# Performance work log

Hardware: AMD Instinct MI355X
Metric: run time of the kernel (lower is better)

The kernel has to match this reference:

```python
import jax, jax.numpy as jnp
import numpy as np

TAU = 0.5

def _l2norm(x, eps=1e-12):
    n = jnp.linalg.norm(x, axis=-1, keepdims=True)
    return x / jnp.maximum(n, eps)

def _gat(a, idx):
    # per-rating gather: a [R, N, ...], idx [R, E] -> [R, E, ...]
    return jax.vmap(lambda x, j: x[j])(a, idx)

def setup_inputs() -> dict:
    key = jax.random.key(0)
    R, Nu, Nm, E, F, d, Dr, OUT = 5, 50000, 20000, 100000, 4, 16, 64, 64
    ks = jax.random.split(key, 17)
    inp = {
        "user_feat_k": jax.random.normal(ks[0], (R, Nu, d), jnp.float32),
        "movie_feat_k": jax.random.normal(ks[1], (R, Nm, d), jnp.float32),
        "user_feat_sum": 0.1 * jax.random.normal(ks[2], (R, Nu, F, d), jnp.float32),
        "movie_feat_sum": 0.1 * jax.random.normal(ks[3], (R, Nm, F, d), jnp.float32),
        "review_feat": 0.1 * jax.random.normal(ks[4], (R, E, F, Dr), jnp.float32),
        "prototypes": 0.1 * jax.random.normal(ks[5], (F, Dr), jnp.float32),
        "eta": jax.random.normal(ks[6], (R, E), jnp.float32),
        "node_w_fwd": 0.25 * jax.random.normal(ks[7], (R, d, d), jnp.float32),
        "review_w_fwd": 0.1 * jax.random.normal(ks[8], (R, d, Dr), jnp.float32),
        "node_w_rev": 0.25 * jax.random.normal(ks[9], (R, d, d), jnp.float32),
        "review_w_rev": 0.1 * jax.random.normal(ks[10], (R, d, Dr), jnp.float32),
        "ufc_w": 0.25 * jax.random.normal(ks[11], (OUT, d), jnp.float32),
        "ufc_b": jnp.zeros((OUT,), jnp.float32),
        "ifc_w": 0.25 * jax.random.normal(ks[12], (OUT, d), jnp.float32),
        "ifc_b": jnp.zeros((OUT,), jnp.float32),
        "edges_u": jax.random.randint(ks[13], (R, E), 0, Nu, jnp.int64),
        "edges_m": jax.random.randint(ks[14], (R, E), 0, Nm, jnp.int64),
        "k": 1,
    }
    return inp

def reference(user_feat_k, movie_feat_k, user_feat_sum, movie_feat_sum,
              review_feat, prototypes, eta, node_w_fwd, review_w_fwd,
              node_w_rev, review_w_rev, ufc_w, ufc_b, ifc_w, ifc_b,
              edges_u, edges_m, k):
    R, E = edges_u.shape
    Nu = user_feat_k.shape[1]
    Nm = movie_feat_k.shape[1]

    # ---- per-edge contrastive weights (vectorized over R ratings) ----
    row_feat = _l2norm(_gat(user_feat_k, edges_u))          # [R,E,d]
    col_feat = _l2norm(_gat(movie_feat_k, edges_m))         # [R,E,d]
    sim_k = (row_feat * col_feat).sum(-1) / TAU             # [R,E]
    sim_all = (_gat(user_feat_sum, edges_u) * _gat(movie_feat_sum, edges_m)).sum(-1) / TAU  # [R,E,F]
    exp_sim = jnp.exp(sim_k) / jnp.exp(sim_all).sum(-1)

    rf_k = review_feat[:, :, k, :]                          # [R,E,Dr]
    ad_k = jnp.einsum('red,d->re', rf_k, prototypes[k]) / TAU
    ad_all = jnp.einsum('refd,fd->ref', review_feat, prototypes) / TAU
    exp_anchor = jnp.exp(ad_k) / jnp.exp(ad_all).sum(-1)

    g = jax.nn.sigmoid(eta[:, :E])                          # eta[rating][:E]
    w = g * exp_anchor + (1.0 - g) * exp_sim                # [R,E]

    # ---- scatter-normalize (fwd + rev etypes give identical w, so the
    #      original's (sum over both)/2 equals a single-direction sum) ----
    norm_user = jax.ops.segment_sum(w.reshape(-1), edges_u.reshape(-1), num_segments=Nu)
    norm_movie = jax.ops.segment_sum(w.reshape(-1), edges_m.reshape(-1), num_segments=Nm)
    n_ij = jnp.sqrt(norm_user[edges_u] * norm_movie[edges_m])  # [R,E]
    w_norm = w / n_ij
    int_dist = w_norm.reshape(R * E, 1)                     # movie->user etypes, rating order

    # ---- GCMC hetero conv: gather src, add projected review feat, scale, scatter ----
    hu = jnp.einsum('rnd,rod->rno', user_feat_k, node_w_fwd)     # node_w per fwd etype
    rfp_f = jnp.einsum('red,rod->reo', rf_k, review_w_fwd)
    msg_m = (_gat(hu, edges_u) + rfp_f) * w_norm[..., None]      # [R,E,d]
    ifeat = jax.ops.segment_sum(msg_m.reshape(R * E, -1), edges_m.reshape(-1), num_segments=Nm)

    hm = jnp.einsum('rnd,rod->rno', movie_feat_k, node_w_rev)    # node_w per rev etype
    rfp_r = jnp.einsum('red,rod->reo', rf_k, review_w_rev)
    msg_u = (_gat(hm, edges_m) + rfp_r) * w_norm[..., None]
    ufeat = jax.ops.segment_sum(msg_u.reshape(R * E, -1), edges_u.reshape(-1), num_segments=Nu)

    lrelu = lambda x: jnp.where(x >= 0, x, 0.1 * x)
    ufeat = lrelu(ufeat) @ ufc_w.T + ufc_b
    ifeat = lrelu(ifeat) @ ifc_w.T + ifc_b
    return (ufeat, ifeat, int_dist)
```

## Files before the change

kernel.cpp:

```cpp
#include <hip/hip_runtime.h>
#include <hip/hip_bf16.h>

#define TAU_INV 2.0f
#define R_ 5
#define NU 50000
#define NM 20000
#define EDGES 100000
#define F_ 4
#define D_ 16
#define DR 64
#define OUT_ 64
#define EPW 32

typedef __attribute__((ext_vector_type(8))) short short8;
typedef __attribute__((ext_vector_type(4))) float f32x4;

__device__ __forceinline__ float dot4(float4 a, float4 b) {
    return a.x * b.x + a.y * b.y + a.z * b.z + a.w * b.w;
}

__device__ __forceinline__ ushort f2bf(float x) {
    __hip_bfloat16 h = __float2bfloat16(x);
    return *reinterpret_cast<ushort*>(&h);
}

__device__ __forceinline__ short8 pack8(float4 lo, float4 hi) {
    short8 v;
    v[0] = (short)f2bf(lo.x); v[1] = (short)f2bf(lo.y);
    v[2] = (short)f2bf(lo.z); v[3] = (short)f2bf(lo.w);
    v[4] = (short)f2bf(hi.x); v[5] = (short)f2bf(hi.y);
    v[6] = (short)f2bf(hi.z); v[7] = (short)f2bf(hi.w);
    return v;
}

__global__ __launch_bounds__(256) void k_edge_w(
    const float* __restrict__ ufk, const float* __restrict__ mfk,
    const float* __restrict__ ufs, const float* __restrict__ mfs,
    const float* __restrict__ rfeat, const float* __restrict__ proto,
    const float* __restrict__ eta, const int* __restrict__ eu,
    const int* __restrict__ em, const int* __restrict__ kp,
    float* __restrict__ wbuf, float* __restrict__ nrm_u, float* __restrict__ nrm_m)
{
    const int tid = threadIdx.x;
    const int wv = tid >> 6, l = tid & 63;
    const int g16 = l >> 4;
    const int j   = l & 15;
    const int r = blockIdx.y;
    int e = (blockIdx.x * 4 + wv) * 4 + g16;
    const bool live = (e < EDGES);
    if (e >= EDGES) e = EDGES - 1;
    const int idx = r * EDGES + e;
    const int u = eu[idx], m = em[idx];
    const int kk = kp[0];

    const float4 pu = ((const float4*)(ufs + (size_t)(r * NU + u) * 64))[j];
    const float4 pm = ((const float4*)(mfs + (size_t)(r * NM + m) * 64))[j];
    float p = dot4(pu, pm);
    p += __shfl_xor(p, 1); p += __shfl_xor(p, 2);
    const float es = expf(p * TAU_INV);
    float dsim = es;
    dsim += __shfl_xor(dsim, 4); dsim += __shfl_xor(dsim, 8);

    const int jc = j & 3;
    const float4 u4 = ((const float4*)(ufk + (size_t)(r * NU + u) * 16))[jc];
    const float4 m4 = ((const float4*)(mfk + (size_t)(r * NM + m) * 16))[jc];
    float su = dot4(u4, u4), sm = dot4(m4, m4), sd = dot4(u4, m4);
    su += __shfl_xor(su, 1); su += __shfl_xor(su, 2);
    sm += __shfl_xor(sm, 1); sm += __shfl_xor(sm, 2);
    sd += __shfl_xor(sd, 1); sd += __shfl_xor(sd, 2);
    const float nsim = expf(sd / (fmaxf(sqrtf(su), 1e-12f) * fmaxf(sqrtf(sm), 1e-12f)) * TAU_INV);

    const float4* rf4 = (const float4*)(rfeat + (size_t)idx * 256);
    const float4* pr4 = (const float4*)proto;
    const int base = (j >> 2) * 16 + (j & 3) * 4;
    float ap = 0.f;
#pragma unroll
    for (int t = 0; t < 4; ++t)
        ap += dot4(rf4[base + t], pr4[base + t]);
    ap += __shfl_xor(ap, 1); ap += __shfl_xor(ap, 2);
    const float ea = expf(ap * TAU_INV);
    float dan = ea;
    dan += __shfl_xor(dan, 4); dan += __shfl_xor(dan, 8);
    const float adk = __shfl(ap, (l & 48) | (kk << 2));
    const float na = expf(adk * TAU_INV);

    const float gt = 1.0f / (1.0f + expf(-eta[idx]));
    const float w = gt * (na / dan) + (1.0f - gt) * (nsim / dsim);

    if (live && j == 0) {
        wbuf[idx] = w;
        atomicAdd(&nrm_u[u], w);
        atomicAdd(&nrm_m[m], w);
    }
}

__global__ __launch_bounds__(256) void k_edge_msg(
    const float* __restrict__ ufk, const float* __restrict__ mfk,
    const float* __restrict__ rfeat,
    const float* __restrict__ nwf, const float* __restrict__ rwf,
    const float* __restrict__ nwr, const float* __restrict__ rwr,
    const int* __restrict__ eu, const int* __restrict__ em, const int* __restrict__ kp,
    const float* __restrict__ wbuf, const float* __restrict__ nrm_u,
    const float* __restrict__ nrm_m,
    float* __restrict__ upre, float* __restrict__ ipre, float* __restrict__ dist_out)
{
    __shared__ __align__(16) ushort s_a[4][EPW][104];

    const int tid = threadIdx.x;
    const int wv = tid >> 6, l = tid & 63;
    const int o = l & 15, q = l >> 4;
    const int r = blockIdx.y;
    const int kk = kp[0];
    const int rE = r * EDGES;

    short8 Bf[3], Br[3];
    {
        const float* wfp = rwf + (size_t)r * 1024 + o * 64;
        const float* wrp = rwr + (size_t)r * 1024 + o * 64;
        const float* nfp = nwf + r * 256 + o * 16;
        const float* nrp = nwr + r * 256 + o * 16;
#pragma unroll
        for (int sl = 0; sl < 2; ++sl) {
            const int bk = 32 * sl + 8 * q;
            Bf[sl] = pack8(*(const float4*)(wfp + bk), *(const float4*)(wfp + bk + 4));
            Br[sl] = pack8(*(const float4*)(wrp + bk), *(const float4*)(wrp + bk + 4));
        }
        const short8 z8 = {0, 0, 0, 0, 0, 0, 0, 0};
        Bf[2] = (q < 2) ? pack8(*(const float4*)(nfp + 8 * q),
                                *(const float4*)(nfp + 8 * q + 4)) : z8;
        Br[2] = (q >= 2) ? pack8(*(const float4*)(nrp + 8 * (q - 2)),
                                 *(const float4*)(nrp + 8 * (q - 2) + 4)) : z8;
    }

    const int ebase = (blockIdx.x * 4 + wv) * EPW;

    int eu32, em32; float wn32;
    {
        int e2 = ebase + (l & 31); if (e2 >= EDGES) e2 = EDGES - 1;
        eu32 = eu[rE + e2]; em32 = em[rE + e2];
        const float w0 = wbuf[rE + e2];
        wn32 = w0 / sqrtf(nrm_u[eu32] * nrm_m[em32]);
    }
    if (l < 32 && ebase + l < EDGES)
        dist_out[rE + ebase + l] = wn32;

    float4 st[12];
#pragma unroll
    for (int t = 0; t < 12; ++t) {
        const int s = l + 64 * t;
        const int j = s / 24;
        const int p = s % 24;
        int e2 = ebase + j; if (e2 >= EDGES) e2 = EDGES - 1;
        const int uj = __shfl(eu32, j);
        const int mj = __shfl(em32, j);
        const float4* src;
        if (p < 16)      src = (const float4*)(rfeat + ((size_t)(rE + e2) * 4 + kk) * 64) + p;
        else if (p < 20) src = (const float4*)(ufk + (size_t)(r * NU + uj) * 16) + (p - 16);
        else             src = (const float4*)(mfk + (size_t)(r * NM + mj) * 16) + (p - 20);
        st[t] = *src;
    }
    char* abase = (char*)&s_a[wv][0][0];
#pragma unroll
    for (int t = 0; t < 12; ++t) {
        const int s = l + 64 * t;
        const int j = s / 24;
        const int p = s % 24;
        uint2 wds;
        wds.x = (uint)f2bf(st[t].x) | ((uint)f2bf(st[t].y) << 16);
        wds.y = (uint)f2bf(st[t].z) | ((uint)f2bf(st[t].w) << 16);
        *(uint2*)(abase + j * 208 + p * 8) = wds;
    }

#pragma unroll
    for (int g = 0; g < 2; ++g) {
        f32x4 accm = {0.f, 0.f, 0.f, 0.f};
        f32x4 accu = {0.f, 0.f, 0.f, 0.f};
        const int row = g * 16 + o;
#pragma unroll
        for (int sl = 0; sl < 3; ++sl) {
            const short8 a = *(const short8*)(abase + row * 208 + (sl * 32 + 8 * q) * 2);
            accm = __builtin_amdgcn_mfma_f32_16x16x32_bf16(a, Bf[sl], accm, 0, 0, 0);
            accu = __builtin_amdgcn_mfma_f32_16x16x32_bf16(a, Br[sl], accu, 0, 0, 0);
        }
#pragma unroll
        for (int i = 0; i < 4; ++i) {
            const int j = g * 16 + q * 4 + i;
            const float wnj = __shfl(wn32, j);
            const int   uj  = __shfl(eu32, j);
            const int   mj  = __shfl(em32, j);
            const bool  livej = (ebase + j) < EDGES;
            const float vm = accm[i] * wnj;
            const float vu = accu[i] * wnj;
            if (livej) {
                atomicAdd(&ipre[(size_t)mj * 16 + o], vm);
                atomicAdd(&upre[(size_t)uj * 16 + o], vu);
            }
        }
    }
}

__global__ __launch_bounds__(256) void k_fc(
    const float* __restrict__ upre, const float* __restrict__ ipre,
    const float* __restrict__ uw, const float* __restrict__ ub,
    const float* __restrict__ iw, const float* __restrict__ ib,
    float* __restrict__ out_u, float* __restrict__ out_i)
{
    const int tid = threadIdx.x;
    const int n = blockIdx.x * 4 + (tid >> 6);
    if (n >= NU + NM) return;
    const int o = tid & 63;
    const float* pre; const float* W; const float* B; float* dst;
    if (n < NU) { pre = upre + (size_t)n * 16; W = uw; B = ub; dst = out_u + (size_t)n * 64; }
    else { int n2 = n - NU; pre = ipre + (size_t)n2 * 16; W = iw; B = ib; dst = out_i + (size_t)n2 * 64; }
    float acc = B[o];
#pragma unroll
    for (int d = 0; d < 16; d++) {
        float x = pre[d];
        x = x >= 0.f ? x : 0.1f * x;
        acc += x * W[o * 16 + d];
    }
    dst[o] = acc;
}

extern "C" void kernel_launch(void* const* d_in, const int* in_sizes, int n_in,
                              void* d_out, int out_size, void* d_ws, size_t ws_size,
                              hipStream_t stream) {
    const float* ufk  = (const float*)d_in[0];
    const float* mfk  = (const float*)d_in[1];
    const float* ufs  = (const float*)d_in[2];
    const float* mfs  = (const float*)d_in[3];
    const float* rfe  = (const float*)d_in[4];
    const float* pro  = (const float*)d_in[5];
    const float* eta  = (const float*)d_in[6];
    const float* nwf  = (const float*)d_in[7];
    const float* rwf  = (const float*)d_in[8];
    const float* nwr  = (const float*)d_in[9];
    const float* rwr  = (const float*)d_in[10];
    const float* uw   = (const float*)d_in[11];
    const float* ub   = (const float*)d_in[12];
    const float* iw   = (const float*)d_in[13];
    const float* ib   = (const float*)d_in[14];
    const int*   eu   = (const int*)d_in[15];
    const int*   em   = (const int*)d_in[16];
    const int*   kp   = (const int*)d_in[17];

    float* out    = (float*)d_out;
    float* out_u  = out;
    float* out_i  = out + (size_t)NU * 64;
    float* out_d  = out_i + (size_t)NM * 64;

    float* ws    = (float*)d_ws;
    float* nrm_u = ws;
    float* nrm_m = nrm_u + NU;
    float* upre  = nrm_m + NM;
    float* ipre  = upre + (size_t)NU * 16;
    float* wbuf  = ipre + (size_t)NM * 16;

    const size_t zeroN = (size_t)NU + NM + (size_t)NU * 16 + (size_t)NM * 16;
    hipMemsetAsync(d_ws, 0, zeroN * sizeof(float), stream);

    dim3 gW((EDGES + 15) / 16, R_);
    k_edge_w<<<gW, 256, 0, stream>>>(ufk, mfk, ufs, mfs, rfe, pro, eta, eu, em, kp,
                                     wbuf, nrm_u, nrm_m);
    dim3 gM((EDGES + 4 * EPW - 1) / (4 * EPW), R_);
    k_edge_msg<<<gM, 256, 0, stream>>>(ufk, mfk, rfe, nwf, rwf, nwr, rwr, eu, em, kp,
                                       wbuf, nrm_u, nrm_m, upre, ipre, out_d);
    k_fc<<<((NU + NM) + 3) / 4, 256, 0, stream>>>(upre, ipre, uw, ub, iw, ib, out_u, out_i);
}
```

Measured before the change: 245.0 us.

## Spill bf16 review slice from weight kernel and read it directly in message kernel

The edge-weight kernel already reads the full review feature row. It now also writes the k-th review slice as packed bf16 into a workspace buffer, when the workspace is large enough. A new message kernel loads MFMA A-fragments straight from that buffer and from the node features, with no LDS staging, so it no longer re-gathers the fp32 review slice. This adds a bf16 write and read of R*E*64 elements and depends on the workspace size, falling back to the old LDS path otherwise. The out-of-range edge clamp in the weight kernel was removed because EDGES divides the grid evenly.

```diff
diff --git a/kernel.cpp b/kernel.cpp
--- a/kernel.cpp
+++ b/kernel.cpp
@@ -6,9 +6,6 @@
 #define NU 50000
 #define NM 20000
 #define EDGES 100000
-#define F_ 4
-#define D_ 16
-#define DR 64
 #define OUT_ 64
 #define EPW 32
 
@@ -18,12 +15,13 @@
 __device__ __forceinline__ float dot4(float4 a, float4 b) {
     return a.x * b.x + a.y * b.y + a.z * b.z + a.w * b.w;
 }
-
 __device__ __forceinline__ ushort f2bf(float x) {
     __hip_bfloat16 h = __float2bfloat16(x);
     return *reinterpret_cast<ushort*>(&h);
 }
-
+__device__ __forceinline__ uint pk2(float a, float b) {
+    return (uint)f2bf(a) | ((uint)f2bf(b) << 16);
+}
 __device__ __forceinline__ short8 pack8(float4 lo, float4 hi) {
     short8 v;
     v[0] = (short)f2bf(lo.x); v[1] = (short)f2bf(lo.y);
@@ -33,22 +31,22 @@
     return v;
 }
 
+template<bool SPILL>
 __global__ __launch_bounds__(256) void k_edge_w(
     const float* __restrict__ ufk, const float* __restrict__ mfk,
     const float* __restrict__ ufs, const float* __restrict__ mfs,
     const float* __restrict__ rfeat, const float* __restrict__ proto,
     const float* __restrict__ eta, const int* __restrict__ eu,
     const int* __restrict__ em, const int* __restrict__ kp,
-    float* __restrict__ wbuf, float* __restrict__ nrm_u, float* __restrict__ nrm_m)
+    float* __restrict__ wbuf, float* __restrict__ nrm_u, float* __restrict__ nrm_m,
+    ushort* __restrict__ msgA)
 {
     const int tid = threadIdx.x;
     const int wv = tid >> 6, l = tid & 63;
     const int g16 = l >> 4;
     const int j   = l & 15;
     const int r = blockIdx.y;
-    int e = (blockIdx.x * 4 + wv) * 4 + g16;
-    const bool live = (e < EDGES);
-    if (e >= EDGES) e = EDGES - 1;
+    const int e = (blockIdx.x * 4 + wv) * 4 + g16;
     const int idx = r * EDGES + e;
     const int u = eu[idx], m = em[idx];
     const int kk = kp[0];
@@ -73,10 +71,10 @@
     const float4* rf4 = (const float4*)(rfeat + (size_t)idx * 256);
     const float4* pr4 = (const float4*)proto;
     const int base = (j >> 2) * 16 + (j & 3) * 4;
-    float ap = 0.f;
-#pragma unroll
-    for (int t = 0; t < 4; ++t)
-        ap += dot4(rf4[base + t], pr4[base + t]);
+    const float4 rr0 = rf4[base + 0], rr1 = rf4[base + 1];
+    const float4 rr2 = rf4[base + 2], rr3 = rf4[base + 3];
+    float ap = dot4(rr0, pr4[base + 0]) + dot4(rr1, pr4[base + 1])
+             + dot4(rr2, pr4[base + 2]) + dot4(rr3, pr4[base + 3]);
     ap += __shfl_xor(ap, 1); ap += __shfl_xor(ap, 2);
     const float ea = expf(ap * TAU_INV);
     float dan = ea;
@@ -87,14 +85,111 @@
     const float gt = 1.0f / (1.0f + expf(-eta[idx]));
     const float w = gt * (na / dan) + (1.0f - gt) * (nsim / dsim);
 
-    if (live && j == 0) {
+    if (j == 0) {
         wbuf[idx] = w;
         atomicAdd(&nrm_u[u], w);
         atomicAdd(&nrm_m[m], w);
     }
-}
-
-__global__ __launch_bounds__(256) void k_edge_msg(
+
+    if (SPILL && (j >> 2) == kk) {
+        uint4 w0, w1;
+        w0.x = pk2(rr0.x, rr0.y); w0.y = pk2(rr0.z, rr0.w);
+        w0.z = pk2(rr1.x, rr1.y); w0.w = pk2(rr1.z, rr1.w);
+        w1.x = pk2(rr2.x, rr2.y); w1.y = pk2(rr2.z, rr2.w);
+        w1.z = pk2(rr3.x, rr3.y); w1.w = pk2(rr3.z, rr3.w);
+        uint4* dst = (uint4*)(msgA + (size_t)idx * 64 + (j & 3) * 16);
+        dst[0] = w0; dst[1] = w1;
+    }
+}
+
+__global__ __launch_bounds__(256) void k_msg_direct(
+    const float* __restrict__ ufk, const float* __restrict__ mfk,
+    const ushort* __restrict__ msgA,
+    const float* __restrict__ nwf, const float* __restrict__ rwf,
+    const float* __restrict__ nwr, const float* __restrict__ rwr,
+    const int* __restrict__ eu, const int* __restrict__ em,
+    const float* __restrict__ wbuf, const float* __restrict__ nrm_u,
+    const float* __restrict__ nrm_m,
+    float* __restrict__ upre, float* __restrict__ ipre, float* __restrict__ dist_out)
+{
+    const int tid = threadIdx.x;
+    const int wv = tid >> 6, l = tid & 63;
+    const int o = l & 15, q = l >> 4;
+    const int r = blockIdx.y;
+    const int rE = r * EDGES;
+
+    short8 Bf[3], Br[3];
+    {
+        const float* wfp = rwf + (size_t)r * 1024 + o * 64;
+        const float* wrp = rwr + (size_t)r * 1024 + o * 64;
+        const float* nfp = nwf + r * 256 + o * 16;
+        const float* nrp = nwr + r * 256 + o * 16;
+#pragma unroll
+        for (int sl = 0; sl < 2; ++sl) {
+            const int bk = 32 * sl + 8 * q;
+            Bf[sl] = pack8(*(const float4*)(wfp + bk), *(const float4*)(wfp + bk + 4));
+            Br[sl] = pack8(*(const float4*)(wrp + bk), *(const float4*)(wrp + bk + 4));
+        }
+        const short8 z8 = {0, 0, 0, 0, 0, 0, 0, 0};
+        Bf[2] = (q < 2) ? pack8(*(const float4*)(nfp + 8 * q),
+                                *(const float4*)(nfp + 8 * q + 4)) : z8;
+        Br[2] = (q >= 2) ? pack8(*(const float4*)(nrp + 8 * (q - 2)),
+                                 *(const float4*)(nrp + 8 * (q - 2) + 4)) : z8;
+    }
+
+    const int ebase = (blockIdx.x * 4 + wv) * EPW;
+
+    int eu32, em32; float wn32;
+    {
+        int e2 = ebase + (l & 31); if (e2 >= EDGES) e2 = EDGES - 1;
+        eu32 = eu[rE + e2]; em32 = em[rE + e2];
+        const float w0 = wbuf[rE + e2];
+        wn32 = w0 / sqrtf(nrm_u[eu32] * nrm_m[em32]);
+    }
+    if (l < 32 && ebase + l < EDGES)
+        dist_out[rE + ebase + l] = wn32;
+
+#pragma unroll
+    for (int g = 0; g < 2; ++g) {
+        const int erow = g * 16 + o;
+        int e2 = ebase + erow; if (e2 >= EDGES) e2 = EDGES - 1;
+        const int u_r = __shfl(eu32, erow);
+        const int m_r = __shfl(em32, erow);
+
+        const char* arow = (const char*)(msgA + (size_t)(rE + e2) * 64);
+        const short8 a0 = *(const short8*)(arow + 0 * 64 + q * 16);
+        const short8 a1 = *(const short8*)(arow + 1 * 64 + q * 16);
+        const float* nb = (q < 2) ? (ufk + (size_t)(r * NU + u_r) * 16 + (q & 1) * 8)
+                                  : (mfk + (size_t)(r * NM + m_r) * 16 + (q & 1) * 8);
+        const short8 a2 = pack8(((const float4*)nb)[0], ((const float4*)nb)[1]);
+
+        f32x4 accm = {0.f, 0.f, 0.f, 0.f};
+        f32x4 accu = {0.f, 0.f, 0.f, 0.f};
+        accm = __builtin_amdgcn_mfma_f32_16x16x32_bf16(a0, Bf[0], accm, 0, 0, 0);
+        accu = __builtin_amdgcn_mfma_f32_16x16x32_bf16(a0, Br[0], accu, 0, 0, 0);
+        accm = __builtin_amdgcn_mfma_f32_16x16x32_bf16(a1, Bf[1], accm, 0, 0, 0);
+        accu = __builtin_amdgcn_mfma_f32_16x16x32_bf16(a1, Br[1], accu, 0, 0, 0);
+        accm = __builtin_amdgcn_mfma_f32_16x16x32_bf16(a2, Bf[2], accm, 0, 0, 0);
+        accu = __builtin_amdgcn_mfma_f32_16x16x32_bf16(a2, Br[2], accu, 0, 0, 0);
+
+#pragma unroll
+        for (int i = 0; i < 4; ++i) {
+            const int j = g * 16 + q * 4 + i;
+            const float wnj = __shfl(wn32, j);
+            const int   uj  = __shfl(eu32, j);
+            const int   mj  = __shfl(em32, j);
+            const bool  livej = (ebase + j) < EDGES;
+            const float vm = accm[i] * wnj;
+            const float vu = accu[i] * wnj;
+            if (livej) {
+                atomicAdd(&ipre[(size_t)mj * 16 + o], vm);
+                atomicAdd(&upre[(size_t)uj * 16 + o], vu);
+            }
+        }
+    }
+}
+
+__global__ __launch_bounds__(256) void k_msg_lds(
     const float* __restrict__ ufk, const float* __restrict__ mfk,
     const float* __restrict__ rfeat,
     const float* __restrict__ nwf, const float* __restrict__ rwf,
@@ -105,7 +200,6 @@
     float* __restrict__ upre, float* __restrict__ ipre, float* __restrict__ dist_out)
 {
     __shared__ __align__(16) ushort s_a[4][EPW][104];
-
     const int tid = threadIdx.x;
     const int wv = tid >> 6, l = tid & 63;
     const int o = l & 15, q = l >> 4;
@@ -133,7 +227,6 @@
     }
 
     const int ebase = (blockIdx.x * 4 + wv) * EPW;
-
     int eu32, em32; float wn32;
     {
         int e2 = ebase + (l & 31); if (e2 >= EDGES) e2 = EDGES - 1;
@@ -148,8 +241,7 @@
 #pragma unroll
     for (int t = 0; t < 12; ++t) {
         const int s = l + 64 * t;
-        const int j = s / 24;
-        const int p = s % 24;
+        const int j = s / 24, p = s % 24;
         int e2 = ebase + j; if (e2 >= EDGES) e2 = EDGES - 1;
         const int uj = __shfl(eu32, j);
         const int mj = __shfl(em32, j);
@@ -163,11 +255,10 @@
 #pragma unroll
     for (int t = 0; t < 12; ++t) {
         const int s = l + 64 * t;
-        const int j = s / 24;
-        const int p = s % 24;
+        const int j = s / 24, p = s % 24;
         uint2 wds;
-        wds.x = (uint)f2bf(st[t].x) | ((uint)f2bf(st[t].y) << 16);
-        wds.y = (uint)f2bf(st[t].z) | ((uint)f2bf(st[t].w) << 16);
+        wds.x = pk2(st[t].x, st[t].y);
+        wds.y = pk2(st[t].z, st[t].w);
         *(uint2*)(abase + j * 208 + p * 8) = wds;
     }
 
@@ -255,15 +346,30 @@
     float* upre  = nrm_m + NM;
     float* ipre  = upre + (size_t)NU * 16;
     float* wbuf  = ipre + (size_t)NM * 16;
+    ushort* msgA = (ushort*)(wbuf + (size_t)R_ * EDGES);
+
+    const size_t baseFloats = (size_t)NU + NM + (size_t)NU * 16 + (size_t)NM * 16
+                            + (size_t)R_ * EDGES;
+    const size_t need = baseFloats * 4 + (size_t)R_ * EDGES * 64 * 2;
+    const bool spill = (ws_size >= need);
 
     const size_t zeroN = (size_t)NU + NM + (size_t)NU * 16 + (size_t)NM * 16;
     hipMemsetAsync(d_ws, 0, zeroN * sizeof(float), stream);
 
     dim3 gW((EDGES + 15) / 16, R_);
-    k_edge_w<<<gW, 256, 0, stream>>>(ufk, mfk, ufs, mfs, rfe, pro, eta, eu, em, kp,
-                                     wbuf, nrm_u, nrm_m);
     dim3 gM((EDGES + 4 * EPW - 1) / (4 * EPW), R_);
-    k_edge_msg<<<gM, 256, 0, stream>>>(ufk, mfk, rfe, nwf, rwf, nwr, rwr, eu, em, kp,
-                                       wbuf, nrm_u, nrm_m, upre, ipre, out_d);
+    if (spill) {
+        k_edge_w<true><<<gW, 256, 0, stream>>>(ufk, mfk, ufs, mfs, rfe, pro, eta,
+                                               eu, em, kp, wbuf, nrm_u, nrm_m, msgA);
+        k_msg_direct<<<gM, 256, 0, stream>>>(ufk, mfk, msgA, nwf, rwf, nwr, rwr,
+                                             eu, em, wbuf, nrm_u, nrm_m,
+                                             upre, ipre, out_d);
+    } else {
+        k_edge_w<false><<<gW, 256, 0, stream>>>(ufk, mfk, ufs, mfs, rfe, pro, eta,
+                                                eu, em, kp, wbuf, nrm_u, nrm_m, msgA);
+        k_msg_lds<<<gM, 256, 0, stream>>>(ufk, mfk, rfe, nwf, rwf, nwr, rwr,
+                                          eu, em, kp, wbuf, nrm_u, nrm_m,
+                                          upre, ipre, out_d);
+    }
     k_fc<<<((NU + NM) + 3) / 4, 256, 0, stream>>>(upre, ipre, uw, ub, iw, ib, out_u, out_i);
 }
```

Measured after the change: 258.4 us. +5.5%, slower.

## Load review features straight to LDS with global_load_lds, 16 edges per wave

Applied to the files above, without the earlier changes.

The message kernel now gives each wave 16 edges instead of 32. It streams the selected review-feature row from global memory directly into LDS as fp32 using the async global_load_lds builtin, and converts to bf16 only when forming the MFMA A fragments. Node features are staged separately in a small bf16 LDS buffer. Edge-count bounds checks are removed because EDGES divides evenly by the per-wave and per-block edge counts. This cuts register staging and conversion work and doubles wave-level parallelism, at the cost of more LDS use and twice as many waves each reloading the weight fragments.

```diff
diff --git a/kernel.cpp b/kernel.cpp
--- a/kernel.cpp
+++ b/kernel.cpp
@@ -6,24 +6,23 @@
 #define NU 50000
 #define NM 20000
 #define EDGES 100000
-#define F_ 4
-#define D_ 16
-#define DR 64
 #define OUT_ 64
-#define EPW 32
 
 typedef __attribute__((ext_vector_type(8))) short short8;
 typedef __attribute__((ext_vector_type(4))) float f32x4;
+typedef __attribute__((address_space(3))) uint  lds_uint;
+typedef const __attribute__((address_space(1))) uint g_uint;
 
 __device__ __forceinline__ float dot4(float4 a, float4 b) {
     return a.x * b.x + a.y * b.y + a.z * b.z + a.w * b.w;
 }
-
 __device__ __forceinline__ ushort f2bf(float x) {
     __hip_bfloat16 h = __float2bfloat16(x);
     return *reinterpret_cast<ushort*>(&h);
 }
-
+__device__ __forceinline__ uint pk2(float a, float b) {
+    return (uint)f2bf(a) | ((uint)f2bf(b) << 16);
+}
 __device__ __forceinline__ short8 pack8(float4 lo, float4 hi) {
     short8 v;
     v[0] = (short)f2bf(lo.x); v[1] = (short)f2bf(lo.y);
@@ -46,9 +45,7 @@
     const int g16 = l >> 4;
     const int j   = l & 15;
     const int r = blockIdx.y;
-    int e = (blockIdx.x * 4 + wv) * 4 + g16;
-    const bool live = (e < EDGES);
-    if (e >= EDGES) e = EDGES - 1;
+    const int e = (blockIdx.x * 4 + wv) * 4 + g16;
     const int idx = r * EDGES + e;
     const int u = eu[idx], m = em[idx];
     const int kk = kp[0];
@@ -87,7 +84,7 @@
     const float gt = 1.0f / (1.0f + expf(-eta[idx]));
     const float w = gt * (na / dan) + (1.0f - gt) * (nsim / dsim);
 
-    if (live && j == 0) {
+    if (j == 0) {
         wbuf[idx] = w;
         atomicAdd(&nrm_u[u], w);
         atomicAdd(&nrm_m[m], w);
@@ -104,7 +101,8 @@
     const float* __restrict__ nrm_m,
     float* __restrict__ upre, float* __restrict__ ipre, float* __restrict__ dist_out)
 {
-    __shared__ __align__(16) ushort s_a[4][EPW][104];
+    __shared__ __align__(16) float  s_rf[4][1280];
+    __shared__ __align__(16) ushort s_nd[4][640];
 
     const int tid = threadIdx.x;
     const int wv = tid >> 6, l = tid & 63;
@@ -112,6 +110,8 @@
     const int r = blockIdx.y;
     const int kk = kp[0];
     const int rE = r * EDGES;
+    const int ebase = (blockIdx.x * 4 + wv) * 16;
+    if (ebase >= EDGES) return;
 
     short8 Bf[3], Br[3];
     {
@@ -132,70 +132,74 @@
                                  *(const float4*)(nrp + 8 * (q - 2) + 4)) : z8;
     }
 
-    const int ebase = (blockIdx.x * 4 + wv) * EPW;
-
-    int eu32, em32; float wn32;
+    int eu16, em16; float wn16;
     {
-        int e2 = ebase + (l & 31); if (e2 >= EDGES) e2 = EDGES - 1;
-        eu32 = eu[rE + e2]; em32 = em[rE + e2];
-        const float w0 = wbuf[rE + e2];
-        wn32 = w0 / sqrtf(nrm_u[eu32] * nrm_m[em32]);
-    }
-    if (l < 32 && ebase + l < EDGES)
-        dist_out[rE + ebase + l] = wn32;
-
-    float4 st[12];
-#pragma unroll
-    for (int t = 0; t < 12; ++t) {
-        const int s = l + 64 * t;
-        const int j = s / 24;
-        const int p = s % 24;
-        int e2 = ebase + j; if (e2 >= EDGES) e2 = EDGES - 1;
-        const int uj = __shfl(eu32, j);
-        const int mj = __shfl(em32, j);
-        const float4* src;
-        if (p < 16)      src = (const float4*)(rfeat + ((size_t)(rE + e2) * 4 + kk) * 64) + p;
-        else if (p < 20) src = (const float4*)(ufk + (size_t)(r * NU + uj) * 16) + (p - 16);
-        else             src = (const float4*)(mfk + (size_t)(r * NM + mj) * 16) + (p - 20);
+        const int e2 = ebase + o;
+        eu16 = eu[rE + e2]; em16 = em[rE + e2];
+        wn16 = wbuf[rE + e2] / sqrtf(nrm_u[eu16] * nrm_m[em16]);
+    }
+    if (l < 16)
+        dist_out[rE + ebase + l] = wn16;
+
+    float* rfw = &s_rf[wv][0];
+#pragma unroll
+    for (int t = 0; t < 5; ++t) {
+        const int s = t * 64 + l;
+        int jj = s / 17, pp = s % 17;
+        if (jj > 15) { jj = 15; pp = 15; }
+        if (pp > 15) pp = 15;
+        const float* gp = rfeat + ((size_t)(rE + ebase + jj) * 4 + kk) * 64 + pp * 4;
+        __builtin_amdgcn_global_load_lds((g_uint*)gp, (lds_uint*)(rfw + t * 256), 16, 0, 0);
+    }
+
+    float4 st[2];
+#pragma unroll
+    for (int t = 0; t < 2; ++t) {
+        const int s = t * 64 + l;
+        const int jj = s >> 3, pp = s & 7;
+        const int uj = __shfl(eu16, jj);
+        const int mj = __shfl(em16, jj);
+        const float4* src = (pp < 4)
+            ? (const float4*)(ufk + (size_t)(r * NU + uj) * 16) + pp
+            : (const float4*)(mfk + (size_t)(r * NM + mj) * 16) + (pp - 4);
         st[t] = *src;
     }
-    char* abase = (char*)&s_a[wv][0][0];
-#pragma unroll
-    for (int t = 0; t < 12; ++t) {
-        const int s = l + 64 * t;
-        const int j = s / 24;
-        const int p = s % 24;
-        uint2 wds;
-        wds.x = (uint)f2bf(st[t].x) | ((uint)f2bf(st[t].y) << 16);
-        wds.y = (uint)f2bf(st[t].z) | ((uint)f2bf(st[t].w) << 16);
-        *(uint2*)(abase + j * 208 + p * 8) = wds;
-    }
-
-#pragma unroll
-    for (int g = 0; g < 2; ++g) {
-        f32x4 accm = {0.f, 0.f, 0.f, 0.f};
-        f32x4 accu = {0.f, 0.f, 0.f, 0.f};
-        const int row = g * 16 + o;
-#pragma unroll
-        for (int sl = 0; sl < 3; ++sl) {
-            const short8 a = *(const short8*)(abase + row * 208 + (sl * 32 + 8 * q) * 2);
-            accm = __builtin_amdgcn_mfma_f32_16x16x32_bf16(a, Bf[sl], accm, 0, 0, 0);
-            accu = __builtin_amdgcn_mfma_f32_16x16x32_bf16(a, Br[sl], accu, 0, 0, 0);
-        }
-#pragma unroll
-        for (int i = 0; i < 4; ++i) {
-            const int j = g * 16 + q * 4 + i;
-            const float wnj = __shfl(wn32, j);
-            const int   uj  = __shfl(eu32, j);
-            const int   mj  = __shfl(em32, j);
-            const bool  livej = (ebase + j) < EDGES;
-            const float vm = accm[i] * wnj;
-            const float vu = accu[i] * wnj;
-            if (livej) {
-                atomicAdd(&ipre[(size_t)mj * 16 + o], vm);
-                atomicAdd(&upre[(size_t)uj * 16 + o], vu);
-            }
-        }
+    char* ndw = (char*)&s_nd[wv][0];
+#pragma unroll
+    for (int t = 0; t < 2; ++t) {
+        const int s = t * 64 + l;
+        const int jj = s >> 3, pp = s & 7;
+        uint2 wd; wd.x = pk2(st[t].x, st[t].y); wd.y = pk2(st[t].z, st[t].w);
+        *(uint2*)(ndw + jj * 80 + pp * 8) = wd;
+    }
+
+    asm volatile("s_waitcnt vmcnt(0)" ::: "memory");
+    __builtin_amdgcn_sched_barrier(0);
+
+    f32x4 accm = {0.f, 0.f, 0.f, 0.f};
+    f32x4 accu = {0.f, 0.f, 0.f, 0.f};
+    const char* rrow = (const char*)rfw + o * 272;
+#pragma unroll
+    for (int sl = 0; sl < 2; ++sl) {
+        const float4* L4 = (const float4*)(rrow + sl * 128 + q * 32);
+        const short8 a = pack8(L4[0], L4[1]);
+        accm = __builtin_amdgcn_mfma_f32_16x16x32_bf16(a, Bf[sl], accm, 0, 0, 0);
+        accu = __builtin_amdgcn_mfma_f32_16x16x32_bf16(a, Br[sl], accu, 0, 0, 0);
+    }
+    {
+        const short8 a = *(const short8*)(ndw + o * 80 + q * 16);
+        accm = __builtin_amdgcn_mfma_f32_16x16x32_bf16(a, Bf[2], accm, 0, 0, 0);
+        accu = __builtin_amdgcn_mfma_f32_16x16x32_bf16(a, Br[2], accu, 0, 0, 0);
+    }
+
+#pragma unroll
+    for (int i = 0; i < 4; ++i) {
+        const int jj = q * 4 + i;
+        const float wnj = __shfl(wn16, jj);
+        const int   uj  = __shfl(eu16, jj);
+        const int   mj  = __shfl(em16, jj);
+        atomicAdd(&ipre[(size_t)mj * 16 + o], accm[i] * wnj);
+        atomicAdd(&upre[(size_t)uj * 16 + o], accu[i] * wnj);
     }
 }
 
@@ -262,7 +266,7 @@
     dim3 gW((EDGES + 15) / 16, R_);
     k_edge_w<<<gW, 256, 0, stream>>>(ufk, mfk, ufs, mfs, rfe, pro, eta, eu, em, kp,
                                      wbuf, nrm_u, nrm_m);
-    dim3 gM((EDGES + 4 * EPW - 1) / (4 * EPW), R_);
+    dim3 gM((EDGES + 63) / 64, R_);
     k_edge_msg<<<gM, 256, 0, stream>>>(ufk, mfk, rfe, nwf, rwf, nwr, rwr, eu, em, kp,
                                        wbuf, nrm_u, nrm_m, upre, ipre, out_d);
     k_fc<<<((NU + NM) + 3) / 4, 256, 0, stream>>>(upre, ipre, uw, ub, iw, ib, out_u, out_i);
```

After: 245.8 us. About the same (+0.3%).
